# Performance work log

Measured on AMD Instinct MI355X. Metric: run time of the kernel, lower is better.

The kernel has to match this reference:

```python
import jax, jax.numpy as jnp
import numpy as np
from jax import lax

DIM = 256; D_STATE = 16; D_CONV = 4; EXPAND = 2
D_INNER = EXPAND * DIM          # 512
DT_RANK = (DIM + 15) // 16      # 16
B, VD, VH, VW = 1, 16, 16, 16


def setup_inputs() -> dict:
    key = jax.random.key(0)
    ks = jax.random.split(key, 20)
    n = lambda k, shape, s=0.02: jax.random.normal(k, shape, dtype=jnp.float32) * s
    A_log = jnp.log(jnp.broadcast_to(jnp.arange(1, D_STATE + 1, dtype=jnp.float32), (D_INNER, D_STATE)))
    return {
        "x": jax.random.normal(ks[0], (B, DIM, VD, VH, VW), dtype=jnp.float32),
        "ln_w": jnp.ones((DIM,), jnp.float32),
        "ln_b": jnp.zeros((DIM,), jnp.float32),
        "in_proj_w": n(ks[1], (2 * D_INNER, DIM)),
        "out_proj_w": n(ks[2], (DIM, D_INNER)),
        "conv_w": n(ks[3], (D_INNER, D_CONV), 0.1),
        "conv_b": jnp.zeros((D_INNER,), jnp.float32),
        "x_proj_w": n(ks[4], (DT_RANK + 2 * D_STATE, D_INNER)),
        "dt_proj_w": n(ks[5], (D_INNER, DT_RANK), 0.1),
        "dt_proj_b": jax.random.uniform(ks[6], (D_INNER,), jnp.float32, -5.0, -3.0),
        "A_log": A_log,
        "D_skip": jnp.ones((D_INNER,), jnp.float32),
        "conv_w_b": n(ks[7], (D_INNER, D_CONV), 0.1),
        "conv_b_b": jnp.zeros((D_INNER,), jnp.float32),
        "x_proj_w_b": n(ks[8], (DT_RANK + 2 * D_STATE, D_INNER)),
        "dt_proj_w_b": n(ks[9], (D_INNER, DT_RANK), 0.1),
        "dt_proj_b_b": jax.random.uniform(ks[10], (D_INNER,), jnp.float32, -5.0, -3.0),
        "A_log_b": A_log,
        "D_skip_b": jnp.ones((D_INNER,), jnp.float32),
    }


def _layernorm(x, w, b, eps=1e-5):
    mu = jnp.mean(x, -1, keepdims=True)
    var = jnp.mean(jnp.square(x - mu), -1, keepdims=True)
    return (x - mu) * lax.rsqrt(var + eps) * w + b


def _ssm_branch(x, conv_w, conv_b, x_proj_w, dt_proj_w, dt_proj_b, A_log, D_skip):
    # x: (B, L, D_INNER). Causal depthwise conv1d + SiLU, then selective scan.
    xt = x.transpose(0, 2, 1)                                    # (B, Din, L)
    xt = lax.conv_general_dilated(xt, conv_w[:, None, :], (1,), [(D_CONV - 1, 0)],
                                  feature_group_count=D_INNER)
    xs = jax.nn.silu(xt + conv_b[:, None]).transpose(0, 2, 1)    # (B, L, Din)
    dbl = xs @ x_proj_w.T                                        # (B, L, dt_rank + 2*Dst)
    dt, Bm, Cm = jnp.split(dbl, [DT_RANK, DT_RANK + D_STATE], axis=-1)
    dt = jax.nn.softplus(dt @ dt_proj_w.T + dt_proj_b)           # (B, L, Din)
    A = -jnp.exp(A_log)                                          # (Din, Dst), negative
    dA = jnp.exp(dt[..., None] * A)                              # (B, L, Din, Dst)
    dBx = dt[..., None] * Bm[:, :, None, :] * xs[..., None]      # (B, L, Din, Dst)

    def step(h, inp):
        dA_t, dBx_t, C_t = inp
        h = dA_t * h + dBx_t                                     # (B, Din, Dst)
        y = jnp.einsum('bds,bs->bd', h, C_t)
        return h, y

    h0 = jnp.zeros((x.shape[0], D_INNER, D_STATE), x.dtype)
    _, ys = lax.scan(step, h0, (dA.transpose(1, 0, 2, 3),
                                dBx.transpose(1, 0, 2, 3),
                                Cm.transpose(1, 0, 2)))
    return ys.transpose(1, 0, 2) + D_skip * xs                   # (B, L, Din)


def _mamba_bi(seq, p):
    # Bidirectional Mamba (bimamba 'Bi'): shared in/out proj, separate scan params.
    xz = seq @ p["in_proj_w"].T
    xb, z = jnp.split(xz, 2, axis=-1)
    y_f = _ssm_branch(xb, p["conv_w"], p["conv_b"], p["x_proj_w"], p["dt_proj_w"],
                      p["dt_proj_b"], p["A_log"], p["D_skip"])
    y_b = _ssm_branch(xb[:, ::-1], p["conv_w_b"], p["conv_b_b"], p["x_proj_w_b"],
                      p["dt_proj_w_b"], p["dt_proj_b_b"], p["A_log_b"], p["D_skip_b"])[:, ::-1]
    y = (y_f + y_b) * jax.nn.silu(z)
    return y @ p["out_proj_w"].T


def _run_dir(x5, p, ln_w, ln_b):
    b, c = x5.shape[:2]
    seq = x5.reshape(b, c, -1).transpose(0, 2, 1)                # (B, L, C)
    seq = _layernorm(seq, ln_w, ln_b)
    y = _mamba_bi(seq, p)
    return y.transpose(0, 2, 1).reshape(x5.shape)


def reference(x, ln_w, ln_b, in_proj_w, out_proj_w, conv_w, conv_b, x_proj_w,
              dt_proj_w, dt_proj_b, A_log, D_skip, conv_w_b, conv_b_b,
              x_proj_w_b, dt_proj_w_b, dt_proj_b_b, A_log_b, D_skip_b):
    p = dict(in_proj_w=in_proj_w, out_proj_w=out_proj_w, conv_w=conv_w, conv_b=conv_b,
             x_proj_w=x_proj_w, dt_proj_w=dt_proj_w, dt_proj_b=dt_proj_b, A_log=A_log,
             D_skip=D_skip, conv_w_b=conv_w_b, conv_b_b=conv_b_b, x_proj_w_b=x_proj_w_b,
             dt_proj_w_b=dt_proj_w_b, dt_proj_b_b=dt_proj_b_b, A_log_b=A_log_b,
             D_skip_b=D_skip_b)
    out_w = _run_dir(x, p, ln_w, ln_b)                                   # w fastest
    out_h = _run_dir(x.transpose(0, 1, 2, 4, 3), p, ln_w, ln_b).transpose(0, 1, 2, 4, 3)
    out_d = _run_dir(x.transpose(0, 1, 3, 4, 2), p, ln_w, ln_b).transpose(0, 1, 4, 2, 3)
    return out_w + out_h + out_d + x
```

## Files before the change

### kernel.cpp

```cpp
#include <hip/hip_runtime.h>
#include <hip/hip_bf16.h>

#define L 4096
#define C 256
#define DIN 512
#define NCH2 128
#define CHUNK2 32
#define LDK 40
#define CST 520

typedef __attribute__((ext_vector_type(8))) short short8;
typedef __attribute__((ext_vector_type(4))) short short4v;
typedef __attribute__((ext_vector_type(4))) float f32x4;
typedef __attribute__((ext_vector_type(2))) float f32x2;


__device__ __forceinline__ int perm_fwd(int dir, int l) {
    if (dir == 0) return l;
    int a = l >> 8, b = (l >> 4) & 15, c = l & 15;
    if (dir == 1) return (a << 8) | (c << 4) | b;
    return (c << 8) | (a << 4) | b;
}

__device__ __forceinline__ float silu_f(float v) { return v / (1.f + __expf(-v)); }

__device__ __forceinline__ float bf2f(short s) {
    unsigned u = ((unsigned)(unsigned short)s) << 16;
    return __builtin_bit_cast(float, u);
}
__device__ __forceinline__ short f2bs(float v) {
    __hip_bfloat16 b = __float2bfloat16(v);
    return __builtin_bit_cast(short, b);
}

__global__ __launch_bounds__(256) void ln_cvt(const float* __restrict__ x,
                                              const float* __restrict__ lnw, const float* __restrict__ lnb,
                                              __hip_bfloat16* __restrict__ ln_bf,
                                              const float* __restrict__ w0, const float* __restrict__ w1,
                                              const float* __restrict__ w2, const float* __restrict__ w3,
                                              const float* __restrict__ w4, const float* __restrict__ w5,
                                              __hip_bfloat16* __restrict__ o0, __hip_bfloat16* __restrict__ o1,
                                              __hip_bfloat16* __restrict__ o2, __hip_bfloat16* __restrict__ o3,
                                              __hip_bfloat16* __restrict__ o4, __hip_bfloat16* __restrict__ o5) {
    int tid = threadIdx.x;
    if (blockIdx.x >= 256) {
        int g = (blockIdx.x - 256) * 256 + tid;
        const float* src; __hip_bfloat16* dst; int idx;
        if (g < 65536)        { src = w0; dst = o0; idx = g; }
        else if (g < 71680)   { src = w1; dst = o1; idx = g - 65536; }
        else if (g < 77824)   { src = w2; dst = o2; idx = g - 71680; }
        else if (g < 110592)  { src = w3; dst = o3; idx = g - 77824; }
        else if (g < 112640)  { src = w4; dst = o4; idx = g - 110592; }
        else                  { src = w5; dst = o5; idx = g - 112640; }
        float4 v = *(const float4*)(src + (size_t)idx * 4);
        dst[(size_t)idx * 4 + 0] = __float2bfloat16(v.x);
        dst[(size_t)idx * 4 + 1] = __float2bfloat16(v.y);
        dst[(size_t)idx * 4 + 2] = __float2bfloat16(v.z);
        dst[(size_t)idx * 4 + 3] = __float2bfloat16(v.w);
        return;
    }
    __shared__ float sS[16][17], sQ[16][17];
    __shared__ float sMu[16], sR[16];
    int pl = tid & 15, cg = tid >> 4;
    int p = blockIdx.x * 16 + pl;
    float v[16];
    float s = 0.f, q = 0.f;
    #pragma unroll
    for (int i = 0; i < 16; ++i) {
        v[i] = x[(size_t)(cg * 16 + i) * L + p];
        s += v[i]; q += v[i] * v[i];
    }
    sS[cg][pl] = s; sQ[cg][pl] = q;
    __syncthreads();
    if (tid < 16) {
        float S = 0.f, Q = 0.f;
        #pragma unroll
        for (int g = 0; g < 16; ++g) { S += sS[g][tid]; Q += sQ[g][tid]; }
        float m = S * (1.f / 256.f);
        float var = Q * (1.f / 256.f) - m * m;
        sMu[tid] = m;
        sR[tid] = rsqrtf(var + 1e-5f);
    }
    __syncthreads();
    float m = sMu[pl], r = sR[pl];
    __hip_bfloat16 ob[16];
    #pragma unroll
    for (int i = 0; i < 16; ++i) {
        int c = cg * 16 + i;
        ob[i] = __float2bfloat16((v[i] - m) * r * lnw[c] + lnb[c]);
    }
    __hip_bfloat16* dst = ln_bf + (size_t)p * C + cg * 16;
    *(short8*)dst = *(short8*)ob;
    *(short8*)(dst + 8) = *(short8*)(ob + 8);
}

__global__ __launch_bounds__(256) void gemm_in(const short* __restrict__ A,
                                               const short* __restrict__ B,
                                               __hip_bfloat16* __restrict__ Cm,
                                               int N, int K) {
    __shared__ __align__(16) short As[64 * LDK];
    __shared__ __align__(16) short Bs[64 * LDK];
    int tid = threadIdx.x;
    int m0 = blockIdx.y * 64, n0 = blockIdx.x * 64;
    int lr = tid >> 2;
    int lk = (tid & 3) * 8;
    int wave = tid >> 6, lane = tid & 63;
    int wm = (wave & 1) * 32, wn = (wave >> 1) * 32;
    int fm = lane & 15;
    int quad = lane >> 4;
    f32x4 acc[2][2] = {};
    const short* Arow = A + (size_t)(m0 + lr) * K + lk;
    const short* Brow = B + (size_t)(n0 + lr) * K + lk;
    for (int kk = 0; kk < K; kk += 32) {
        short8 av = *(const short8*)(Arow + kk);
        short8 bv = *(const short8*)(Brow + kk);
        __syncthreads();
        *(short8*)(As + lr * LDK + lk) = av;
        *(short8*)(Bs + lr * LDK + lk) = bv;
        __syncthreads();
        short8 af0 = *(const short8*)(As + (wm + fm) * LDK + quad * 8);
        short8 af1 = *(const short8*)(As + (wm + 16 + fm) * LDK + quad * 8);
        short8 bf0 = *(const short8*)(Bs + (wn + fm) * LDK + quad * 8);
        short8 bf1 = *(const short8*)(Bs + (wn + 16 + fm) * LDK + quad * 8);
        acc[0][0] = __builtin_amdgcn_mfma_f32_16x16x32_bf16(af0, bf0, acc[0][0], 0, 0, 0);
        acc[0][1] = __builtin_amdgcn_mfma_f32_16x16x32_bf16(af0, bf1, acc[0][1], 0, 0, 0);
        acc[1][0] = __builtin_amdgcn_mfma_f32_16x16x32_bf16(af1, bf0, acc[1][0], 0, 0, 0);
        acc[1][1] = __builtin_amdgcn_mfma_f32_16x16x32_bf16(af1, bf1, acc[1][1], 0, 0, 0);
    }
    int col = lane & 15;
    int rowb = quad * 4;
    #pragma unroll
    for (int j = 0; j < 2; ++j) {
        int n = n0 + wn + j * 16 + col;
        #pragma unroll
        for (int i = 0; i < 2; ++i) {
            #pragma unroll
            for (int r = 0; r < 4; ++r) {
                int m = m0 + wm + i * 16 + rowb + r;
                Cm[(size_t)m * N + n] = __float2bfloat16(acc[i][j][r]);
            }
        }
    }
}

__global__ __launch_bounds__(512, 6) void conv_xproj_dt(const __hip_bfloat16* __restrict__ xz,
                                                     const float* __restrict__ cw_f, const float* __restrict__ cb_f,
                                                     const float* __restrict__ cw_b, const float* __restrict__ cb_b,
                                                     const short* __restrict__ B0, const short* __restrict__ B1,
                                                     const short* __restrict__ Wd0, const short* __restrict__ Wd1,
                                                     const float* __restrict__ dtb0, const float* __restrict__ dtb1,
                                                     float* __restrict__ dbl_out,
                                                     short* __restrict__ dt_tl,
                                                     short* __restrict__ xs_tl,
                                                     float* __restrict__ sumH,
                                                     float* __restrict__ sdt_arr) {
    int z = blockIdx.y;
    const short* xzs = (const short*)xz;
    const short* Bb = z ? B1 : B0;
    const short* Wd = z ? Wd1 : Wd0;
    const float* dtb = z ? dtb1 : dtb0;
    const float* cw = z ? cw_b : cw_f;
    const float* cb = z ? cb_b : cb_f;
    float* Cb = dbl_out + (size_t)z * 12288 * 48;
    int tid = threadIdx.x;
    int m0 = blockIdx.x * 32;
    int dir = m0 >> 12;
    int i0 = m0 & 4095;
    int bd = z ? (3 + dir) : dir;
    __shared__ __align__(16) short uni[35 * 512];
    __shared__ __align__(16) short As[32 * LDK];
    __shared__ __align__(16) float sB[32 * 16];
    int u0 = z ? (4064 - i0) : (i0 - 3);
    #pragma unroll
    for (int it = 0; it < 5; ++it) {
        int idx = it * 512 + tid;
        if (idx < 2240) {
            int r = idx >> 6;
            int c8 = idx & 63;
            int u = u0 + r;
            short8 v = {};
            if (u >= 0 && u < 4096) {
                int p = perm_fwd(dir, u);
                v = *(const short8*)(xzs + (size_t)p * 1024 + c8 * 8);
            }
            *(short8*)(uni + r * 512 + c8 * 8) = v;
        }
    }
    __syncthreads();
    short8 cv[4];
    {
        int d0 = tid;
        float4 w4 = *(const float4*)(cw + d0 * 4);
        float bias = cb[d0];
        #pragma unroll
        for (int tg = 0; tg < 4; ++tg) {
            float wv[11];
            int rbase = z ? (24 - tg * 8) : (tg * 8);
            #pragma unroll
            for (int r = 0; r < 11; ++r)
                wv[r] = bf2f(uni[(rbase + r) * 512 + d0]);
            short8 o;
            #pragma unroll
            for (int j = 0; j < 8; ++j) {
                float a = bias;
                if (z) {
                    a = fmaf(w4.w, wv[7 - j + 0], a);
                    a = fmaf(w4.z, wv[7 - j + 1], a);
                    a = fmaf(w4.y, wv[7 - j + 2], a);
                    a = fmaf(w4.x, wv[7 - j + 3], a);
                } else {
                    a = fmaf(w4.x, wv[j + 0], a);
                    a = fmaf(w4.y, wv[j + 1], a);
                    a = fmaf(w4.z, wv[j + 2], a);
                    a = fmaf(w4.w, wv[j + 3], a);
                }
                o[j] = f2bs(silu_f(a));
            }
            cv[tg] = o;
            size_t gbase = (((size_t)bd * L + i0) >> 3) + tg;
            *(short8*)(xs_tl + gbase * 4096 + (size_t)d0 * 8) = o;
        }
    }
    __syncthreads();
    {
        int d0 = tid;
        #pragma unroll
        for (int tg = 0; tg < 4; ++tg) {
            short8 o = cv[tg];
            #pragma unroll
            for (int j = 0; j < 8; ++j)
                uni[(tg * 8 + j) * CST + d0] = o[j];
        }
    }
    __syncthreads();
    int wave = tid >> 6, lane = tid & 63;
    int wn = wave * 16;
    int fm = lane & 15;
    int quad = lane >> 4;
    f32x4 acc[2] = {};
    if (wn < 48) {
        const short* Bfrag = Bb + (size_t)(wn + fm) * DIN + quad * 8;
        #pragma unroll
        for (int kk = 0; kk < DIN; kk += 32) {
            short8 bf  = *(const short8*)(Bfrag + kk);
            short8 af0 = *(const short8*)(uni + fm * CST + kk + quad * 8);
            short8 af1 = *(const short8*)(uni + (16 + fm) * CST + kk + quad * 8);
            acc[0] = __builtin_amdgcn_mfma_f32_16x16x32_bf16(af0, bf, acc[0], 0, 0, 0);
            acc[1] = __builtin_amdgcn_mfma_f32_16x16x32_bf16(af1, bf, acc[1], 0, 0, 0);
        }
    }
    int col = lane & 15;
    int rowb = quad * 4;
    if (wn < 48) {
        #pragma unroll
        for (int i = 0; i < 2; ++i) {
            #pragma unroll
            for (int r = 0; r < 4; ++r) {
                int m = m0 + i * 16 + rowb + r;
                Cb[(size_t)m * 48 + wn + col] = acc[i][r];
            }
        }
    }
    if (wave == 1) {
        #pragma unroll
        for (int i = 0; i < 2; ++i) {
            #pragma unroll
            for (int r = 0; r < 4; ++r)
                sB[(i * 16 + rowb + r) * 16 + col] = acc[i][r];
        }
    }
    __syncthreads();
    if (wave == 0) {
        #pragma unroll
        for (int i = 0; i < 2; ++i) {
            int row = i * 16 + rowb;
            #pragma unroll
            for (int r = 0; r < 4; ++r)
                As[(row + r) * LDK + col] = f2bs(acc[i][r]);
        }
    }
    if (tid < 256) {
        int rr = tid >> 3, k2 = 16 + (tid & 7) * 2;
        *(int*)(As + rr * LDK + k2) = 0;
    }
    __syncthreads();
    short8 afd[2];
    afd[0] = *(const short8*)(As + fm * LDK + quad * 8);
    afd[1] = *(const short8*)(As + (16 + fm) * LDK + quad * 8);
    int nbase = wave * 64;
    short8 zz8 = {};
    #pragma unroll
    for (int nt = 0; nt < 4; ++nt) {
        int nnl = nbase + nt * 16;
        short8 bfd = zz8;
        if (quad < 2) bfd = *(const short8*)(Wd + (size_t)(nnl + fm) * 16 + quad * 8);
        f32x4 ad[2] = {};
        ad[0] = __builtin_amdgcn_mfma_f32_16x16x32_bf16(afd[0], bfd, ad[0], 0, 0, 0);
        ad[1] = __builtin_amdgcn_mfma_f32_16x16x32_bf16(afd[1], bfd, ad[1], 0, 0, 0);
        int n = nnl + col;
        float bn = dtb[n];
        #pragma unroll
        for (int i = 0; i < 2; ++i) {
            size_t grow = (size_t)z * 12288 + m0 + i * 16 + rowb;
            size_t g = grow >> 3;
            int off = (int)(grow & 7);
            short4v o4;
            #pragma unroll
            for (int r = 0; r < 4; ++r) {
                float v = ad[i][r] + bn;
                float sp = (v > 20.f) ? v : __logf(1.f + __expf(v));
                o4[r] = f2bs(sp);
            }
            *(short4v*)(dt_tl + g * 4096 + (size_t)n * 8 + off) = o4;
            #pragma unroll
            for (int r = 0; r < 4; ++r)
                uni[(i * 16 + rowb + r) * CST + n] = o4[r];
        }
    }
    __syncthreads();
    {
        int ch = i0 >> 5;
        int d = tid;
        f32x2 h2s[8];
        #pragma unroll
        for (int i = 0; i < 8; ++i) h2s[i] = (f32x2){0.f, 0.f};
        float sdt = 0.f;
        #pragma unroll
        for (int tg = 0; tg < 4; ++tg) {
            short8 xv8 = cv[tg];
            #pragma unroll
            for (int j = 0; j < 8; ++j) {
                int t = tg * 8 + j;
                const float* brow = sB + t * 16;
                float dt = bf2f(uni[t * CST + d]);
                float dx = dt * bf2f(xv8[j]);
                float e1 = __expf(-dt);
                float e2 = e1 * e1;
                float e4 = e2 * e2;
                float e8 = e4 * e4;
                f32x2 p[8];
                p[0] = (f32x2){e1, e2};
                f32x2 q2 = (f32x2){e2, e2};
                f32x2 q4 = (f32x2){e4, e4};
                f32x2 q8 = (f32x2){e8, e8};
                p[1] = p[0] * q2;
                p[2] = p[0] * q4;
                p[3] = p[1] * q4;
                p[4] = p[0] * q8;
                p[5] = p[1] * q8;
                p[6] = p[2] * q8;
                p[7] = p[3] * q8;
                f32x2 dx2 = (f32x2){dx, dx};
                sdt += dt;
                #pragma unroll
                for (int i = 0; i < 4; ++i) {
                    f32x4 B4 = *(const f32x4*)(brow + 4 * i);
                    h2s[2 * i]     = p[2 * i]     * h2s[2 * i]     + dx2 * (f32x2){B4[0], B4[1]};
                    h2s[2 * i + 1] = p[2 * i + 1] * h2s[2 * i + 1] + dx2 * (f32x2){B4[2], B4[3]};
                }
            }
        }
        size_t o = ((size_t)(bd * NCH2 + ch) * DIN + d) * 16;
        #pragma unroll
        for (int i = 0; i < 4; ++i) {
            f32x4 v = {h2s[2 * i].x, h2s[2 * i].y, h2s[2 * i + 1].x, h2s[2 * i + 1].y};
            *(f32x4*)(sumH + o + 4 * i) = v;
        }
        sdt_arr[((size_t)bd * NCH2 + ch) * DIN + d] = sdt;
    }
}

__global__ __launch_bounds__(256) void scan_passB(float* __restrict__ sumH,
                                                  const float* __restrict__ sdt_arr) {
    int g = blockIdx.x * 256 + threadIdx.x;
    int bd = g >> 13;
    int r = g & 8191;
    int d = r >> 4;
    float As = -(float)((r & 15) + 1);
    float gst = 0.f;
    size_t hbase = ((size_t)bd * NCH2) << 13;
    size_t sbase = (size_t)bd * NCH2 * DIN;
    for (int cb = 0; cb < NCH2; cb += 8) {
        float hv[8], pv[8];
        #pragma unroll
        for (int k = 0; k < 8; ++k) {
            hv[k] = sumH[hbase + ((size_t)(cb + k) << 13) + r];
            pv[k] = sdt_arr[sbase + (size_t)(cb + k) * DIN + d];
        }
        #pragma unroll
        for (int k = 0; k < 8; ++k)
            pv[k] = __expf(As * pv[k]);
        #pragma unroll
        for (int k = 0; k < 8; ++k) {
            sumH[hbase + ((size_t)(cb + k) << 13) + r] = gst;
            gst = fmaf(pv[k], gst, hv[k]);
        }
    }
}

__global__ __launch_bounds__(256) void scan_passC(const short* __restrict__ xs_tl,
                                                  const short* __restrict__ dt_tl,
                                                  const float* __restrict__ dbl_all,
                                                  const float* __restrict__ Dsk_f,
                                                  const float* __restrict__ Dsk_b,
                                                  const float* __restrict__ Hin,
                                                  short* __restrict__ y_fl) {
    __shared__ __align__(16) float sdbl[CHUNK2 * 48];
    int tid = threadIdx.x;
    int ch = blockIdx.x;
    int bd = blockIdx.y;
    int d = blockIdx.z * 256 + tid;
    int br = bd / 3;
    const float* Dsk  = br ? Dsk_b  : Dsk_f;
    {
        const float4* src = (const float4*)(dbl_all + ((size_t)bd * L + ch * CHUNK2) * 48);
        float4* dst = (float4*)sdbl;
        dst[tid] = src[tid];
        if (tid < 128) dst[256 + tid] = src[256 + tid];
    }
    f32x2 h2[8];
    size_t o = ((size_t)(bd * NCH2 + ch) * DIN + d) * 16;
    #pragma unroll
    for (int i = 0; i < 8; ++i)
        h2[i] = (f32x2){Hin[o + 2 * i], Hin[o + 2 * i + 1]};
    float Dv = Dsk[d];
    size_t g0 = ((size_t)bd * L + ch * CHUNK2) >> 3;
    short* yrow = y_fl + ((size_t)bd * L + ch * CHUNK2) * DIN + d;
    __syncthreads();
    for (int jo = 0; jo < CHUNK2; jo += 8) {
        short8 xv8 = *(const short8*)(xs_tl + (g0 + (jo >> 3)) * 4096 + (size_t)d * 8);
        short8 dt8 = *(const short8*)(dt_tl + (g0 + (jo >> 3)) * 4096 + (size_t)d * 8);
        #pragma unroll
        for (int j = 0; j < 8; ++j) {
            const float* row = sdbl + (jo + j) * 48;
            float dt = bf2f(dt8[j]);
            float xv = bf2f(xv8[j]);
            float dx = dt * xv;
            float e1 = __expf(-dt);
            float e2 = e1 * e1;
            float e4 = e2 * e2;
            float e8 = e4 * e4;
            f32x2 p[8];
            p[0] = (f32x2){e1, e2};
            f32x2 q2 = (f32x2){e2, e2};
            f32x2 q4 = (f32x2){e4, e4};
            f32x2 q8 = (f32x2){e8, e8};
            p[1] = p[0] * q2;
            p[2] = p[0] * q4;
            p[3] = p[1] * q4;
            p[4] = p[0] * q8;
            p[5] = p[1] * q8;
            p[6] = p[2] * q8;
            p[7] = p[3] * q8;
            f32x2 dx2 = (f32x2){dx, dx};
            f32x2 y2 = (f32x2){0.f, 0.f};
            #pragma unroll
            for (int i = 0; i < 4; ++i) {
                f32x4 B4 = *(const f32x4*)(row + 16 + 4 * i);
                f32x4 C4 = *(const f32x4*)(row + 32 + 4 * i);
                h2[2 * i]     = p[2 * i]     * h2[2 * i]     + dx2 * (f32x2){B4[0], B4[1]};
                y2 = y2 + h2[2 * i] * (f32x2){C4[0], C4[1]};
                h2[2 * i + 1] = p[2 * i + 1] * h2[2 * i + 1] + dx2 * (f32x2){B4[2], B4[3]};
                y2 = y2 + h2[2 * i + 1] * (f32x2){C4[2], C4[3]};
            }
            float y = fmaf(Dv, xv, y2.x + y2.y);
            yrow[(size_t)(jo + j) * DIN] = f2bs(y);
        }
    }
}

__global__ __launch_bounds__(256) void gemm_out_final(const short* __restrict__ y_bf,
                                                      const short* __restrict__ xz_bf,
                                                      const short* __restrict__ W,
                                                      const float* __restrict__ x,
                                                      float* __restrict__ out) {
    __shared__ __align__(16) short As[96 * LDK];
    __shared__ __align__(16) short Bs[128 * LDK];
    int tid = threadIdx.x;
    int g = blockIdx.x;
    int n00 = blockIdx.y * 128;
    int r0 = tid >> 3;
    int ka = (tid & 7) * 4;
    int jj = r0 >> 4, w = r0 & 15;
    int dh = g * 2 + jj;
    int d = dh >> 4, h = dh & 15;
    int p = (d << 8) | (h << 4) | w;
    int lD[3];
    lD[0] = (d << 8) | (h << 4) | w;
    lD[1] = (d << 8) | (w << 4) | h;
    lD[2] = (h << 8) | (w << 4) | d;
    const short* yfr[3]; const short* ybr[3];
    #pragma unroll
    for (int D = 0; D < 3; ++D) {
        yfr[D] = y_bf + ((size_t)D * L + lD[D]) * DIN + ka;
        ybr[D] = y_bf + ((size_t)(3 + D) * L + (4095 - lD[D])) * DIN + ka;
    }
    const short* zr = xz_bf + (size_t)p * 1024 + 512 + ka;
    int br0 = tid >> 2;
    int kb = (tid & 3) * 8;
    const short* Brow0 = W + (size_t)(n00 + br0) * DIN + kb;
    const short* Brow1 = W + (size_t)(n00 + br0 + 64) * DIN + kb;
    int wave = tid >> 6, lane = tid & 63;
    int wn = wave * 32;
    int fm = lane & 15;
    int quad = lane >> 4;
    f32x4 acc[6][2] = {};
    for (int kk = 0; kk < DIN; kk += 32) {
        short4v z4 = *(const short4v*)(zr + kk);
        float sz0 = silu_f(bf2f(z4[0]));
        float sz1 = silu_f(bf2f(z4[1]));
        float sz2 = silu_f(bf2f(z4[2]));
        float sz3 = silu_f(bf2f(z4[3]));
        short8 bv0 = *(const short8*)(Brow0 + kk);
        short8 bv1 = *(const short8*)(Brow1 + kk);
        short4v gv[3];
        #pragma unroll
        for (int D = 0; D < 3; ++D) {
            short4v yf4 = *(const short4v*)(yfr[D] + kk);
            short4v yb4 = *(const short4v*)(ybr[D] + kk);
            gv[D][0] = f2bs((bf2f(yf4[0]) + bf2f(yb4[0])) * sz0);
            gv[D][1] = f2bs((bf2f(yf4[1]) + bf2f(yb4[1])) * sz1);
            gv[D][2] = f2bs((bf2f(yf4[2]) + bf2f(yb4[2])) * sz2);
            gv[D][3] = f2bs((bf2f(yf4[3]) + bf2f(yb4[3])) * sz3);
        }
        __syncthreads();
        *(short4v*)(As + r0 * LDK + ka) = gv[0];
        *(short4v*)(As + (r0 + 32) * LDK + ka) = gv[1];
        *(short4v*)(As + (r0 + 64) * LDK + ka) = gv[2];
        *(short8*)(Bs + br0 * LDK + kb) = bv0;
        *(short8*)(Bs + (br0 + 64) * LDK + kb) = bv1;
        __syncthreads();
        #pragma unroll
        for (int nj = 0; nj < 2; ++nj) {
            short8 bf = *(const short8*)(Bs + (wn + nj * 16 + fm) * LDK + quad * 8);
            #pragma unroll
            for (int mi = 0; mi < 6; ++mi) {
                short8 af = *(const short8*)(As + (mi * 16 + fm) * LDK + quad * 8);
                acc[mi][nj] = __builtin_amdgcn_mfma_f32_16x16x32_bf16(af, bf, acc[mi][nj], 0, 0, 0);
            }
        }
    }
    int col = lane & 15;
    int rowb = quad * 4;
    #pragma unroll
    for (int nj = 0; nj < 2; ++nj) {
        int c = n00 + wn + nj * 16 + col;
        #pragma unroll
        for (int j2 = 0; j2 < 2; ++j2) {
            f32x4 s = acc[0 + j2][nj] + acc[2 + j2][nj] + acc[4 + j2][nj];
            size_t off = (size_t)c * L + (size_t)(g * 2 + j2) * 16 + rowb;
            float4 xv = *(const float4*)(x + off);
            float4 ov;
            ov.x = xv.x + s[0];
            ov.y = xv.y + s[1];
            ov.z = xv.z + s[2];
            ov.w = xv.w + s[3];
            *(float4*)(out + off) = ov;
        }
    }
}

extern "C" void kernel_launch(void* const* d_in, const int* in_sizes, int n_in,
                              void* d_out, int out_size, void* d_ws, size_t ws_size,
                              hipStream_t stream) {
    const float* x          = (const float*)d_in[0];
    const float* ln_w       = (const float*)d_in[1];
    const float* ln_b       = (const float*)d_in[2];
    const float* in_proj_w  = (const float*)d_in[3];
    const float* out_proj_w = (const float*)d_in[4];
    const float* conv_w     = (const float*)d_in[5];
    const float* conv_b     = (const float*)d_in[6];
    const float* x_proj_w   = (const float*)d_in[7];
    const float* dt_proj_w  = (const float*)d_in[8];
    const float* dt_proj_b  = (const float*)d_in[9];
    const float* A_log      = (const float*)d_in[10];
    const float* D_skip     = (const float*)d_in[11];
    const float* conv_w_b   = (const float*)d_in[12];
    const float* conv_b_b   = (const float*)d_in[13];
    const float* x_proj_w_b = (const float*)d_in[14];
    const float* dt_proj_w_b= (const float*)d_in[15];
    const float* dt_proj_b_b= (const float*)d_in[16];
    const float* A_log_b    = (const float*)d_in[17];
    const float* D_skip_b   = (const float*)d_in[18];
    float* out = (float*)d_out;
    (void)A_log; (void)A_log_b;

    float* ws = (float*)d_ws;
    float* dbl_all = ws;
    float* sumH    = dbl_all + (size_t)6 * L * 48;
    float* sdt_arr = sumH + (size_t)6 * NCH2 * DIN * 16;
    __hip_bfloat16* ln_bf   = (__hip_bfloat16*)(sdt_arr + (size_t)6 * NCH2 * DIN);
    __hip_bfloat16* xz_bf   = ln_bf + (size_t)L * C;
    short* xs_tl = (short*)(xz_bf + (size_t)L * 1024);
    short* dt_tl = xs_tl + (size_t)6 * L * DIN;
    short* y_fl  = dt_tl + (size_t)6 * L * DIN;
    __hip_bfloat16* w_in_bf = (__hip_bfloat16*)(y_fl + (size_t)6 * L * DIN);
    __hip_bfloat16* w_xp_bf = w_in_bf + 262144;
    __hip_bfloat16* w_xpb_bf= w_xp_bf + 24576;
    __hip_bfloat16* w_out_bf= w_xpb_bf + 24576;
    __hip_bfloat16* w_dt_bf = w_out_bf + 131072;
    __hip_bfloat16* w_dtb_bf= w_dt_bf + 8192;

    ln_cvt<<<704, 256, 0, stream>>>(x, ln_w, ln_b, ln_bf,
                                    in_proj_w, x_proj_w, x_proj_w_b, out_proj_w,
                                    dt_proj_w, dt_proj_w_b,
                                    w_in_bf, w_xp_bf, w_xpb_bf, w_out_bf, w_dt_bf, w_dtb_bf);

    gemm_in<<<dim3(16, 64), 256, 0, stream>>>((const short*)ln_bf, (const short*)w_in_bf,
                                              xz_bf, 1024, C);

    conv_xproj_dt<<<dim3(384, 2), 512, 0, stream>>>(xz_bf, conv_w, conv_b, conv_w_b, conv_b_b,
                                                    (const short*)w_xp_bf, (const short*)w_xpb_bf,
                                                    (const short*)w_dt_bf, (const short*)w_dtb_bf,
                                                    dt_proj_b, dt_proj_b_b,
                                                    dbl_all, dt_tl, xs_tl, sumH, sdt_arr);

    scan_passB<<<192, 256, 0, stream>>>(sumH, sdt_arr);
    scan_passC<<<dim3(NCH2, 6, 2), 256, 0, stream>>>(xs_tl, dt_tl, dbl_all, D_skip, D_skip_b,
                                                     sumH, y_fl);

    gemm_out_final<<<dim3(128, 2), 256, 0, stream>>>(y_fl, (const short*)xz_bf,
                                                     (const short*)w_out_bf, x, out);
}
```

Before: 196.7 us.

## Fuse layernorm into in-projection GEMM and convert weights to bf16 on the fly

Removes the separate ln_cvt kernel. The layernorm is now computed inside a new gemm_in_ln kernel, which keeps the normalized 64-row tile in shared memory and runs a 64x256 tile per block, reading the fp32 weights directly from global memory and converting them to bf16 in registers. The other GEMM kernels also read fp32 weights and convert them in place. This saves one launch and the round trips of the ln_bf and converted-weight buffers, but it doubles weight read bandwidth, repeats the conversion in every block, and loads the B operand without shared-memory staging. The grid shrinks to 256 blocks with more work each, and x is re-read once per N-tile.

```diff
diff --git a/kernel.cpp b/kernel.cpp
--- a/kernel.cpp
+++ b/kernel.cpp
@@ -8,6 +8,7 @@
 #define CHUNK2 32
 #define LDK 40
 #define CST 520
+#define AST 264
 
 typedef __attribute__((ext_vector_type(8))) short short8;
 typedef __attribute__((ext_vector_type(4))) short short4v;
@@ -32,112 +33,90 @@
     __hip_bfloat16 b = __float2bfloat16(v);
     return __builtin_bit_cast(short, b);
 }
-
-__global__ __launch_bounds__(256) void ln_cvt(const float* __restrict__ x,
-                                              const float* __restrict__ lnw, const float* __restrict__ lnb,
-                                              __hip_bfloat16* __restrict__ ln_bf,
-                                              const float* __restrict__ w0, const float* __restrict__ w1,
-                                              const float* __restrict__ w2, const float* __restrict__ w3,
-                                              const float* __restrict__ w4, const float* __restrict__ w5,
-                                              __hip_bfloat16* __restrict__ o0, __hip_bfloat16* __restrict__ o1,
-                                              __hip_bfloat16* __restrict__ o2, __hip_bfloat16* __restrict__ o3,
-                                              __hip_bfloat16* __restrict__ o4, __hip_bfloat16* __restrict__ o5) {
-    int tid = threadIdx.x;
-    if (blockIdx.x >= 256) {
-        int g = (blockIdx.x - 256) * 256 + tid;
-        const float* src; __hip_bfloat16* dst; int idx;
-        if (g < 65536)        { src = w0; dst = o0; idx = g; }
-        else if (g < 71680)   { src = w1; dst = o1; idx = g - 65536; }
-        else if (g < 77824)   { src = w2; dst = o2; idx = g - 71680; }
-        else if (g < 110592)  { src = w3; dst = o3; idx = g - 77824; }
-        else if (g < 112640)  { src = w4; dst = o4; idx = g - 110592; }
-        else                  { src = w5; dst = o5; idx = g - 112640; }
-        float4 v = *(const float4*)(src + (size_t)idx * 4);
-        dst[(size_t)idx * 4 + 0] = __float2bfloat16(v.x);
-        dst[(size_t)idx * 4 + 1] = __float2bfloat16(v.y);
-        dst[(size_t)idx * 4 + 2] = __float2bfloat16(v.z);
-        dst[(size_t)idx * 4 + 3] = __float2bfloat16(v.w);
-        return;
-    }
+__device__ __forceinline__ short8 cvt8(const float* p) {
+    float4 a = *(const float4*)p;
+    float4 b = *(const float4*)(p + 4);
+    short8 o;
+    o[0] = f2bs(a.x); o[1] = f2bs(a.y); o[2] = f2bs(a.z); o[3] = f2bs(a.w);
+    o[4] = f2bs(b.x); o[5] = f2bs(b.y); o[6] = f2bs(b.z); o[7] = f2bs(b.w);
+    return o;
+}
+
+__global__ __launch_bounds__(256) void gemm_in_ln(const float* __restrict__ x,
+                                                  const float* __restrict__ lnw,
+                                                  const float* __restrict__ lnb,
+                                                  const float* __restrict__ Bw,
+                                                  __hip_bfloat16* __restrict__ Cm) {
+    __shared__ __align__(16) short As[64 * AST];
     __shared__ float sS[16][17], sQ[16][17];
     __shared__ float sMu[16], sR[16];
+    int tid = threadIdx.x;
+    int m0 = blockIdx.y * 64, n0 = blockIdx.x * 256;
     int pl = tid & 15, cg = tid >> 4;
-    int p = blockIdx.x * 16 + pl;
-    float v[16];
-    float s = 0.f, q = 0.f;
-    #pragma unroll
-    for (int i = 0; i < 16; ++i) {
-        v[i] = x[(size_t)(cg * 16 + i) * L + p];
-        s += v[i]; q += v[i] * v[i];
-    }
-    sS[cg][pl] = s; sQ[cg][pl] = q;
-    __syncthreads();
-    if (tid < 16) {
-        float S = 0.f, Q = 0.f;
-        #pragma unroll
-        for (int g = 0; g < 16; ++g) { S += sS[g][tid]; Q += sQ[g][tid]; }
-        float m = S * (1.f / 256.f);
-        float var = Q * (1.f / 256.f) - m * m;
-        sMu[tid] = m;
-        sR[tid] = rsqrtf(var + 1e-5f);
-    }
-    __syncthreads();
-    float m = sMu[pl], r = sR[pl];
-    __hip_bfloat16 ob[16];
-    #pragma unroll
-    for (int i = 0; i < 16; ++i) {
-        int c = cg * 16 + i;
-        ob[i] = __float2bfloat16((v[i] - m) * r * lnw[c] + lnb[c]);
-    }
-    __hip_bfloat16* dst = ln_bf + (size_t)p * C + cg * 16;
-    *(short8*)dst = *(short8*)ob;
-    *(short8*)(dst + 8) = *(short8*)(ob + 8);
-}
-
-__global__ __launch_bounds__(256) void gemm_in(const short* __restrict__ A,
-                                               const short* __restrict__ B,
-                                               __hip_bfloat16* __restrict__ Cm,
-                                               int N, int K) {
-    __shared__ __align__(16) short As[64 * LDK];
-    __shared__ __align__(16) short Bs[64 * LDK];
-    int tid = threadIdx.x;
-    int m0 = blockIdx.y * 64, n0 = blockIdx.x * 64;
-    int lr = tid >> 2;
-    int lk = (tid & 3) * 8;
+    #pragma unroll
+    for (int pp = 0; pp < 4; ++pp) {
+        int p = m0 + pp * 16 + pl;
+        float v[16];
+        float s = 0.f, q = 0.f;
+        #pragma unroll
+        for (int i = 0; i < 16; ++i) {
+            v[i] = x[(size_t)(cg * 16 + i) * L + p];
+            s += v[i]; q += v[i] * v[i];
+        }
+        sS[cg][pl] = s; sQ[cg][pl] = q;
+        __syncthreads();
+        if (tid < 16) {
+            float S = 0.f, Q = 0.f;
+            #pragma unroll
+            for (int g = 0; g < 16; ++g) { S += sS[g][tid]; Q += sQ[g][tid]; }
+            float m = S * (1.f / 256.f);
+            float var = Q * (1.f / 256.f) - m * m;
+            sMu[tid] = m;
+            sR[tid] = rsqrtf(var + 1e-5f);
+        }
+        __syncthreads();
+        float m = sMu[pl], r = sR[pl];
+        short ob[16];
+        #pragma unroll
+        for (int i = 0; i < 16; ++i) {
+            int c = cg * 16 + i;
+            ob[i] = f2bs((v[i] - m) * r * lnw[c] + lnb[c]);
+        }
+        short* dst = As + (pp * 16 + pl) * AST + cg * 16;
+        *(short8*)dst = *(short8*)ob;
+        *(short8*)(dst + 8) = *(short8*)(ob + 8);
+        __syncthreads();
+    }
     int wave = tid >> 6, lane = tid & 63;
-    int wm = (wave & 1) * 32, wn = (wave >> 1) * 32;
+    int wn = n0 + wave * 64;
     int fm = lane & 15;
     int quad = lane >> 4;
-    f32x4 acc[2][2] = {};
-    const short* Arow = A + (size_t)(m0 + lr) * K + lk;
-    const short* Brow = B + (size_t)(n0 + lr) * K + lk;
-    for (int kk = 0; kk < K; kk += 32) {
-        short8 av = *(const short8*)(Arow + kk);
-        short8 bv = *(const short8*)(Brow + kk);
-        __syncthreads();
-        *(short8*)(As + lr * LDK + lk) = av;
-        *(short8*)(Bs + lr * LDK + lk) = bv;
-        __syncthreads();
-        short8 af0 = *(const short8*)(As + (wm + fm) * LDK + quad * 8);
-        short8 af1 = *(const short8*)(As + (wm + 16 + fm) * LDK + quad * 8);
-        short8 bf0 = *(const short8*)(Bs + (wn + fm) * LDK + quad * 8);
-        short8 bf1 = *(const short8*)(Bs + (wn + 16 + fm) * LDK + quad * 8);
-        acc[0][0] = __builtin_amdgcn_mfma_f32_16x16x32_bf16(af0, bf0, acc[0][0], 0, 0, 0);
-        acc[0][1] = __builtin_amdgcn_mfma_f32_16x16x32_bf16(af0, bf1, acc[0][1], 0, 0, 0);
-        acc[1][0] = __builtin_amdgcn_mfma_f32_16x16x32_bf16(af1, bf0, acc[1][0], 0, 0, 0);
-        acc[1][1] = __builtin_amdgcn_mfma_f32_16x16x32_bf16(af1, bf1, acc[1][1], 0, 0, 0);
+    f32x4 acc[4][4] = {};
+    #pragma unroll
+    for (int kk = 0; kk < 256; kk += 32) {
+        short8 af[4];
+        #pragma unroll
+        for (int mi = 0; mi < 4; ++mi)
+            af[mi] = *(const short8*)(As + (mi * 16 + fm) * AST + kk + quad * 8);
+        #pragma unroll
+        for (int nt = 0; nt < 4; ++nt) {
+            short8 bf = cvt8(Bw + (size_t)(wn + nt * 16 + fm) * 256 + kk + quad * 8);
+            #pragma unroll
+            for (int mi = 0; mi < 4; ++mi)
+                acc[mi][nt] = __builtin_amdgcn_mfma_f32_16x16x32_bf16(af[mi], bf, acc[mi][nt], 0, 0, 0);
+        }
     }
     int col = lane & 15;
     int rowb = quad * 4;
     #pragma unroll
-    for (int j = 0; j < 2; ++j) {
-        int n = n0 + wn + j * 16 + col;
-        #pragma unroll
-        for (int i = 0; i < 2; ++i) {
+    for (int nt = 0; nt < 4; ++nt) {
+        int n = wn + nt * 16 + col;
+        #pragma unroll
+        for (int mi = 0; mi < 4; ++mi) {
             #pragma unroll
             for (int r = 0; r < 4; ++r) {
-                int m = m0 + wm + i * 16 + rowb + r;
-                Cm[(size_t)m * N + n] = __float2bfloat16(acc[i][j][r]);
+                int m = m0 + mi * 16 + rowb + r;
+                Cm[(size_t)m * 1024 + n] = __float2bfloat16(acc[mi][nt][r]);
             }
         }
     }
@@ -146,8 +125,8 @@
 __global__ __launch_bounds__(512, 6) void conv_xproj_dt(const __hip_bfloat16* __restrict__ xz,
                                                      const float* __restrict__ cw_f, const float* __restrict__ cb_f,
                                                      const float* __restrict__ cw_b, const float* __restrict__ cb_b,
-                                                     const short* __restrict__ B0, const short* __restrict__ B1,
-                                                     const short* __restrict__ Wd0, const short* __restrict__ Wd1,
+                                                     const float* __restrict__ B0, const float* __restrict__ B1,
+                                                     const float* __restrict__ Wd0, const float* __restrict__ Wd1,
                                                      const float* __restrict__ dtb0, const float* __restrict__ dtb1,
                                                      float* __restrict__ dbl_out,
                                                      short* __restrict__ dt_tl,
@@ -156,8 +135,8 @@
                                                      float* __restrict__ sdt_arr) {
     int z = blockIdx.y;
     const short* xzs = (const short*)xz;
-    const short* Bb = z ? B1 : B0;
-    const short* Wd = z ? Wd1 : Wd0;
+    const float* Bb = z ? B1 : B0;
+    const float* Wd = z ? Wd1 : Wd0;
     const float* dtb = z ? dtb1 : dtb0;
     const float* cw = z ? cw_b : cw_f;
     const float* cb = z ? cb_b : cb_f;
@@ -239,10 +218,10 @@
     int quad = lane >> 4;
     f32x4 acc[2] = {};
     if (wn < 48) {
-        const short* Bfrag = Bb + (size_t)(wn + fm) * DIN + quad * 8;
+        const float* Bfrag = Bb + (size_t)(wn + fm) * DIN + quad * 8;
         #pragma unroll
         for (int kk = 0; kk < DIN; kk += 32) {
-            short8 bf  = *(const short8*)(Bfrag + kk);
+            short8 bf  = cvt8(Bfrag + kk);
             short8 af0 = *(const short8*)(uni + fm * CST + kk + quad * 8);
             short8 af1 = *(const short8*)(uni + (16 + fm) * CST + kk + quad * 8);
             acc[0] = __builtin_amdgcn_mfma_f32_16x16x32_bf16(af0, bf, acc[0], 0, 0, 0);
@@ -293,7 +272,7 @@
     for (int nt = 0; nt < 4; ++nt) {
         int nnl = nbase + nt * 16;
         short8 bfd = zz8;
-        if (quad < 2) bfd = *(const short8*)(Wd + (size_t)(nnl + fm) * 16 + quad * 8);
+        if (quad < 2) bfd = cvt8(Wd + (size_t)(nnl + fm) * 16 + quad * 8);
         f32x4 ad[2] = {};
         ad[0] = __builtin_amdgcn_mfma_f32_16x16x32_bf16(afd[0], bfd, ad[0], 0, 0, 0);
         ad[1] = __builtin_amdgcn_mfma_f32_16x16x32_bf16(afd[1], bfd, ad[1], 0, 0, 0);
@@ -471,7 +450,7 @@
 
 __global__ __launch_bounds__(256) void gemm_out_final(const short* __restrict__ y_bf,
                                                       const short* __restrict__ xz_bf,
-                                                      const short* __restrict__ W,
+                                                      const float* __restrict__ W,
                                                       const float* __restrict__ x,
                                                       float* __restrict__ out) {
     __shared__ __align__(16) short As[96 * LDK];
@@ -498,8 +477,8 @@
     const short* zr = xz_bf + (size_t)p * 1024 + 512 + ka;
     int br0 = tid >> 2;
     int kb = (tid & 3) * 8;
-    const short* Brow0 = W + (size_t)(n00 + br0) * DIN + kb;
-    const short* Brow1 = W + (size_t)(n00 + br0 + 64) * DIN + kb;
+    const float* Brow0 = W + (size_t)(n00 + br0) * DIN + kb;
+    const float* Brow1 = W + (size_t)(n00 + br0 + 64) * DIN + kb;
     int wave = tid >> 6, lane = tid & 63;
     int wn = wave * 32;
     int fm = lane & 15;
@@ -511,8 +490,8 @@
         float sz1 = silu_f(bf2f(z4[1]));
         float sz2 = silu_f(bf2f(z4[2]));
         float sz3 = silu_f(bf2f(z4[3]));
-        short8 bv0 = *(const short8*)(Brow0 + kk);
-        short8 bv1 = *(const short8*)(Brow1 + kk);
+        short8 bv0 = cvt8(Brow0 + kk);
+        short8 bv1 = cvt8(Brow1 + kk);
         short4v gv[3];
         #pragma unroll
         for (int D = 0; D < 3; ++D) {
@@ -589,29 +568,16 @@
     float* dbl_all = ws;
     float* sumH    = dbl_all + (size_t)6 * L * 48;
     float* sdt_arr = sumH + (size_t)6 * NCH2 * DIN * 16;
-    __hip_bfloat16* ln_bf   = (__hip_bfloat16*)(sdt_arr + (size_t)6 * NCH2 * DIN);
-    __hip_bfloat16* xz_bf   = ln_bf + (size_t)L * C;
+    __hip_bfloat16* xz_bf   = (__hip_bfloat16*)(sdt_arr + (size_t)6 * NCH2 * DIN);
     short* xs_tl = (short*)(xz_bf + (size_t)L * 1024);
     short* dt_tl = xs_tl + (size_t)6 * L * DIN;
     short* y_fl  = dt_tl + (size_t)6 * L * DIN;
-    __hip_bfloat16* w_in_bf = (__hip_bfloat16*)(y_fl + (size_t)6 * L * DIN);
-    __hip_bfloat16* w_xp_bf = w_in_bf + 262144;
-    __hip_bfloat16* w_xpb_bf= w_xp_bf + 24576;
-    __hip_bfloat16* w_out_bf= w_xpb_bf + 24576;
-    __hip_bfloat16* w_dt_bf = w_out_bf + 131072;
-    __hip_bfloat16* w_dtb_bf= w_dt_bf + 8192;
-
-    ln_cvt<<<704, 256, 0, stream>>>(x, ln_w, ln_b, ln_bf,
-                                    in_proj_w, x_proj_w, x_proj_w_b, out_proj_w,
-                                    dt_proj_w, dt_proj_w_b,
-                                    w_in_bf, w_xp_bf, w_xpb_bf, w_out_bf, w_dt_bf, w_dtb_bf);
-
-    gemm_in<<<dim3(16, 64), 256, 0, stream>>>((const short*)ln_bf, (const short*)w_in_bf,
-                                              xz_bf, 1024, C);
+
+    gemm_in_ln<<<dim3(4, 64), 256, 0, stream>>>(x, ln_w, ln_b, in_proj_w, xz_bf);
 
     conv_xproj_dt<<<dim3(384, 2), 512, 0, stream>>>(xz_bf, conv_w, conv_b, conv_w_b, conv_b_b,
-                                                    (const short*)w_xp_bf, (const short*)w_xpb_bf,
-                                                    (const short*)w_dt_bf, (const short*)w_dtb_bf,
+                                                    x_proj_w, x_proj_w_b,
+                                                    dt_proj_w, dt_proj_w_b,
                                                     dt_proj_b, dt_proj_b_b,
                                                     dbl_all, dt_tl, xs_tl, sumH, sdt_arr);
 
@@ -620,5 +586,5 @@
                                                      sumH, y_fl);
 
     gemm_out_final<<<dim3(128, 2), 256, 0, stream>>>(y_fl, (const short*)xz_bf,
-                                                     (const short*)w_out_bf, x, out);
-}
+                                                     out_proj_w, x, out);
+}
```

Measured after the change: 213.1 us. +8.4%, slower.
